# Optimization experiments

Hardware: AMD Instinct MI355X
Metric: run time of the kernel (lower is better)

## Reference

```python
import jax, jax.numpy as jnp
import numpy as np

B, S, E, L = 4, 4096, 1024, 64
SCALE = float(np.sqrt(L))


def setup_inputs() -> dict:
    key = jax.random.key(0)
    ks = jax.random.split(key, 7)
    x = jax.random.normal(ks[0], (B, S, E), dtype=jnp.float32)
    # causal mask: positions with mask==0 are disallowed (masked_fill semantics)
    mask = jnp.tril(jnp.ones((S, S), dtype=jnp.int32))
    # Linear params (torch Linear: y = x @ W.T + b); store as [E, L] for x @ W
    sd = 1.0 / np.sqrt(E)
    Wq = jax.random.uniform(ks[1], (E, L), jnp.float32, -sd, sd)
    Wk = jax.random.uniform(ks[2], (E, L), jnp.float32, -sd, sd)
    Wv = jax.random.uniform(ks[3], (E, L), jnp.float32, -sd, sd)
    bq = jax.random.uniform(ks[4], (L,), jnp.float32, -sd, sd)
    bk = jax.random.uniform(ks[5], (L,), jnp.float32, -sd, sd)
    bv = jax.random.uniform(ks[6], (L,), jnp.float32, -sd, sd)
    return {"x": x, "Wq": Wq, "Wk": Wk, "Wv": Wv,
            "bq": bq, "bk": bk, "bv": bv, "mask": mask}


def reference(x, Wq, Wk, Wv, bq, bk, bv, mask):
    # Q,K,V: [B, S, L]
    Q = x @ Wq + bq
    K = x @ Wk + bk
    V = x @ Wv + bv
    # scores: [B, S, S] -- naive full matrix, faithful to the original
    scores = jnp.einsum('bsl,btl->bst', Q, K) / SCALE
    scores = jnp.where(mask == 0, -jnp.inf, scores)
    attn = jax.nn.softmax(scores, axis=-1)
    return jnp.einsum('bst,btl->bsl', attn, V)
```

## Files before the change

### kernel.cpp

```cpp
#include <hip/hip_runtime.h>
#include <hip/hip_bf16.h>
#include <cstdint>

typedef __bf16 bf16_t;
typedef __bf16 bf16x8 __attribute__((ext_vector_type(8)));
typedef float f32x4 __attribute__((ext_vector_type(4)));

#define B_ 4
#define S_ 4096
#define E_ 1024
#define L_ 64

__device__ __forceinline__ f32x4 mfma16(bf16x8 a, bf16x8 b, f32x4 c) {
  return __builtin_amdgcn_mfma_f32_16x16x32_bf16(a, b, c, 0, 0, 0);
}

template <int CTRL>
__device__ __forceinline__ float dpp_max_step(float x) {
  int t = __builtin_amdgcn_update_dpp(0, __float_as_int(x), CTRL, 0xF, 0xF, true);
  return fmaxf(x, __int_as_float(t));
}
template <int CTRL>
__device__ __forceinline__ float dpp_add_step(float x) {
  int t = __builtin_amdgcn_update_dpp(0, __float_as_int(x), CTRL, 0xF, 0xF, true);
  return x + __int_as_float(t);
}
__device__ __forceinline__ float dpp_reduce_max16(float x) {
  x = dpp_max_step<0x121>(x);
  x = dpp_max_step<0x122>(x);
  x = dpp_max_step<0x124>(x);
  x = dpp_max_step<0x128>(x);
  return x;
}
__device__ __forceinline__ float dpp_reduce_add16(float x) {
  x = dpp_add_step<0x121>(x);
  x = dpp_add_step<0x122>(x);
  x = dpp_add_step<0x124>(x);
  x = dpp_add_step<0x128>(x);
  return x;
}


__global__ void prep_w_kernel(const float* __restrict__ Wq, const float* __restrict__ Wk,
                              const float* __restrict__ Wv, bf16_t* __restrict__ Wf) {
  int n = blockIdx.x;
  const float* W = (n < 64) ? Wq : (n < 128 ? Wk : Wv);
  int col = n & 63;
  int nt = n >> 4, lr = n & 15;
  for (int k = threadIdx.x; k < E_; k += blockDim.x) {
    int kt = k >> 5, lg = (k >> 3) & 3, e = k & 7;
    Wf[((size_t)((nt * 32 + kt) * 64 + lg * 16 + lr) << 3) + e] = (bf16_t)W[(size_t)k * L_ + col];
  }
}

__global__ __launch_bounds__(512) void qkv_proj_kernel(
    const float* __restrict__ x, const bf16_t* __restrict__ Wf,
    const float* __restrict__ bq, const float* __restrict__ bk, const float* __restrict__ bv,
    bf16_t* __restrict__ Qf, bf16_t* __restrict__ Kf, bf16_t* __restrict__ Vf) {
  __shared__ __align__(16) bf16_t xs[2][32][136];

  const int tid = threadIdx.x;
  const int w = tid >> 6, l = tid & 63;
  const int lr = l & 15, lg = l >> 4;
  const int rowgrp = w & 1, colgrp = w >> 1;
  const int m0b = blockIdx.x * 32;
  const int srow = tid >> 4, scol = (tid & 15) * 8;

  f32x4 acc[3];
#pragma unroll
  for (int t = 0; t < 3; ++t) acc[t] = f32x4{0.f, 0.f, 0.f, 0.f};

  const float* xsrc = x + (size_t)(m0b + srow) * E_ + scol;

  {
    float4 u0 = *reinterpret_cast<const float4*>(xsrc);
    float4 u1 = *reinterpret_cast<const float4*>(xsrc + 4);
    bf16x8 pk;
    pk[0] = (bf16_t)u0.x; pk[1] = (bf16_t)u0.y; pk[2] = (bf16_t)u0.z; pk[3] = (bf16_t)u0.w;
    pk[4] = (bf16_t)u1.x; pk[5] = (bf16_t)u1.y; pk[6] = (bf16_t)u1.z; pk[7] = (bf16_t)u1.w;
    *reinterpret_cast<bf16x8*>(&xs[0][srow][scol]) = pk;
  }
  float4 v0 = *reinterpret_cast<const float4*>(xsrc + 128);
  float4 v1 = *reinterpret_cast<const float4*>(xsrc + 132);
  __syncthreads();

  int buf = 0;
  for (int it = 0; it < 8; ++it) {
    if (it + 1 < 8) {
      bf16x8 pk;
      pk[0] = (bf16_t)v0.x; pk[1] = (bf16_t)v0.y; pk[2] = (bf16_t)v0.z; pk[3] = (bf16_t)v0.w;
      pk[4] = (bf16_t)v1.x; pk[5] = (bf16_t)v1.y; pk[6] = (bf16_t)v1.z; pk[7] = (bf16_t)v1.w;
      *reinterpret_cast<bf16x8*>(&xs[buf ^ 1][srow][scol]) = pk;
    }
    if (it + 2 < 8) {
      v0 = *reinterpret_cast<const float4*>(xsrc + (it + 2) * 128);
      v1 = *reinterpret_cast<const float4*>(xsrc + (it + 2) * 128 + 4);
    }
    const bf16_t* xr = &xs[buf][rowgrp * 16 + lr][0];
#pragma unroll
    for (int ks = 0; ks < 4; ++ks) {
      bf16x8 a = *reinterpret_cast<const bf16x8*>(xr + ks * 32 + lg * 8);
      const int kt = it * 4 + ks;
#pragma unroll
      for (int t = 0; t < 3; ++t) {
        const int nt = colgrp * 3 + t;
        bf16x8 b = *reinterpret_cast<const bf16x8*>(Wf + (((size_t)(nt * 32 + kt) * 64 + l) << 3));
        acc[t] = mfma16(a, b, acc[t]);
      }
    }
    __syncthreads();
    buf ^= 1;
  }

#pragma unroll
  for (int t = 0; t < 3; ++t) {
    int ng = colgrp * 48 + t * 16 + lr;
    int mat = ng >> 6;
    int ncol = ng & 63;
    const float* bias = (mat == 0) ? bq : (mat == 1 ? bk : bv);
    float bb = bias[ncol];
    const int ktq = ncol >> 5, lgw = (ncol >> 3) & 3, ew = ncol & 7;
    const int vt = ncol >> 4, lrw_v = ncol & 15;
#pragma unroll
    for (int r = 0; r < 4; ++r) {
      int mg = m0b + rowgrp * 16 + lg * 4 + r;
      float v = acc[t][r] + bb;
      if (mat < 2) {
        int rt = mg >> 4, lrw = mg & 15;
        size_t idx = (((size_t)((rt * 2 + ktq) * 64 + lgw * 16 + lrw)) << 3) + ew;
        if (mat == 0) Qf[idx] = (bf16_t)v; else Kf[idx] = (bf16_t)v;
      } else {
        int batch = mg >> 12, sl = mg & (S_ - 1);
        int st = sl >> 5, lgv = (sl >> 3) & 3, ev = sl & 7;
        Vf[((size_t)batch << 18) + (((size_t)((st * 4 + vt) * 64 + lgv * 16 + lrw_v)) << 3) + ev] = (bf16_t)v;
      }
    }
  }
}

__global__ __launch_bounds__(256) void attn_kernel(
    const bf16_t* __restrict__ Qf, const bf16_t* __restrict__ Kf,
    const bf16_t* __restrict__ Vf, float* __restrict__ Opart, float* __restrict__ mlpart) {
  __shared__ __align__(16) bf16_t p_lds[4][16 * 72];
  __shared__ bf16_t od_lds[3][16][68];
  __shared__ float ml_lds[3][16][2];

  const int c = threadIdx.x >> 6, l = threadIdx.x & 63;
  const int lr = l & 15, lg = l >> 4;
  const int u = blockIdx.x;
  const int batch = u & 3;
  const int strip = (u >> 2) & 3;
  const int h = (u >> 4) & 1;
  const int qt = 63 - (u >> 5);
  const int qsi = ((u >> 5) << 4) | (u & 15);
  const int qrow = qt * 64 + strip * 16;
  const size_t qbase = (size_t)batch * S_ + qrow;
  bf16_t* pw = p_lds[c];

  const int rtq = batch * 256 + qt * 4 + strip;
  bf16x8 qa0 = *reinterpret_cast<const bf16x8*>(Qf + (((size_t)(rtq * 2) * 64 + l) << 3));
  bf16x8 qa1 = *reinterpret_cast<const bf16x8*>(Qf + (((size_t)(rtq * 2 + 1) * 64 + l) << 3));
  const bf16_t* Vb = Vf + ((size_t)batch << 18);

  f32x4 o[4];
  float m[4], ssum[4];
#pragma unroll
  for (int rr = 0; rr < 4; ++rr) { o[rr] = f32x4{0.f, 0.f, 0.f, 0.f}; m[rr] = -1e30f; ssum[rr] = 0.f; }

  for (int kt = 2 * c + h; kt <= qt; kt += 8) {
    const int t0 = kt * 64;
    f32x4 st[4];
#pragma unroll
    for (int cf = 0; cf < 4; ++cf) st[cf] = f32x4{0.f, 0.f, 0.f, 0.f};
#pragma unroll
    for (int cf = 0; cf < 4; ++cf) {
      const int rtk = batch * 256 + kt * 4 + cf;
      bf16x8 b0 = *reinterpret_cast<const bf16x8*>(Kf + (((size_t)(rtk * 2) * 64 + l) << 3));
      bf16x8 b1 = *reinterpret_cast<const bf16x8*>(Kf + (((size_t)(rtk * 2 + 1) * 64 + l) << 3));
      st[cf] = mfma16(qa0, b0, st[cf]);
      st[cf] = mfma16(qa1, b1, st[cf]);
    }
    const bool diag = (kt == qt);
    float p[4][4];
#pragma unroll
    for (int rr = 0; rr < 4; ++rr) {
      const int qg = qrow + lg * 4 + rr;
      float rowmax = -1e30f;
#pragma unroll
      for (int cf = 0; cf < 4; ++cf) {
        float s = st[cf][rr] * 0.125f;
        if (diag && (t0 + cf * 16 + lr) > qg) s = -1e30f;
        p[cf][rr] = s;
        rowmax = fmaxf(rowmax, s);
      }
      rowmax = dpp_reduce_max16(rowmax);
      float mnew = fmaxf(m[rr], rowmax);
      float scale = __expf(m[rr] - mnew);
      float rs = 0.f;
#pragma unroll
      for (int cf = 0; cf < 4; ++cf) {
        float e = __expf(p[cf][rr] - mnew);
        p[cf][rr] = e;
        rs += e;
      }
      rs = dpp_reduce_add16(rs);
      ssum[rr] = ssum[rr] * scale + rs;
#pragma unroll
      for (int cf = 0; cf < 4; ++cf) o[cf][rr] *= scale;
      m[rr] = mnew;
    }
#pragma unroll
    for (int rr = 0; rr < 4; ++rr)
#pragma unroll
      for (int cf = 0; cf < 4; ++cf)
        pw[(lg * 4 + rr) * 72 + cf * 16 + lr] = (bf16_t)p[cf][rr];
    bf16x8 pa0 = *reinterpret_cast<const bf16x8*>(pw + lr * 72 + lg * 8);
    bf16x8 pa1 = *reinterpret_cast<const bf16x8*>(pw + lr * 72 + 32 + lg * 8);
    const int st0 = kt * 2;
#pragma unroll
    for (int cf = 0; cf < 4; ++cf) {
      bf16x8 v0 = *reinterpret_cast<const bf16x8*>(Vb + (((size_t)((st0 * 4 + cf) * 64 + l)) << 3));
      bf16x8 v1 = *reinterpret_cast<const bf16x8*>(Vb + (((size_t)(((st0 + 1) * 4 + cf) * 64 + l)) << 3));
      o[cf] = mfma16(pa0, v0, o[cf]);
      o[cf] = mfma16(pa1, v1, o[cf]);
    }
  }

  if (c > 0) {
    if (lr == 0) {
#pragma unroll
      for (int rr = 0; rr < 4; ++rr) {
        ml_lds[c - 1][lg * 4 + rr][0] = m[rr];
        ml_lds[c - 1][lg * 4 + rr][1] = ssum[rr];
      }
    }
#pragma unroll
    for (int cf = 0; cf < 4; ++cf)
#pragma unroll
      for (int rr = 0; rr < 4; ++rr)
        od_lds[c - 1][lg * 4 + rr][cf * 16 + lr] = (bf16_t)o[cf][rr];
  }
  __syncthreads();
  if (c == 0) {
    float* Op = Opart + (size_t)(h * 1024 + qsi) * 1024;
    float* mlp = mlpart + (size_t)(h * 1024 + qsi) * 32;
#pragma unroll
    for (int rr = 0; rr < 4; ++rr) {
      const int row = lg * 4 + rr;
      float M = m[rr];
      float mv[3];
#pragma unroll
      for (int cc = 0; cc < 3; ++cc) {
        mv[cc] = ml_lds[cc][row][0];
        M = fmaxf(M, mv[cc]);
      }
      float f0 = __expf(m[rr] - M);
      float Lsum = ssum[rr] * f0;
      float fc[3];
#pragma unroll
      for (int cc = 0; cc < 3; ++cc) {
        fc[cc] = __expf(mv[cc] - M);
        Lsum += ml_lds[cc][row][1] * fc[cc];
      }
      if (lr == 0) { mlp[row * 2] = M; mlp[row * 2 + 1] = Lsum; }
#pragma unroll
      for (int cf = 0; cf < 4; ++cf) {
        float val = o[cf][rr] * f0;
#pragma unroll
        for (int cc = 0; cc < 3; ++cc)
          val += (float)od_lds[cc][row][cf * 16 + lr] * fc[cc];
        Op[row * 64 + cf * 16 + lr] = val;
      }
    }
  }
}

__global__ __launch_bounds__(64) void combine_kernel(
    const float* __restrict__ Opart, const float* __restrict__ mlpart,
    float* __restrict__ out) {
  const int b = blockIdx.x;
  const int batch = b & 3, strip = (b >> 2) & 3, qt = 63 - (b >> 4);
  const int l = threadIdx.x;
  const int row = l >> 2, c0 = (l & 3) * 16;
  const float* ml0 = mlpart + ((size_t)(0 * 1024 + b) * 16 + row) * 2;
  const float* ml1 = mlpart + ((size_t)(1 * 1024 + b) * 16 + row) * 2;
  float m0 = ml0[0], l0 = ml0[1], m1 = ml1[0], l1 = ml1[1];
  float M = fmaxf(m0, m1);
  float f0 = __expf(m0 - M), f1 = __expf(m1 - M);
  float inv = 1.f / (l0 * f0 + l1 * f1);
  const float* O0 = Opart + (size_t)(0 * 1024 + b) * 1024 + row * 64 + c0;
  const float* O1 = Opart + (size_t)(1 * 1024 + b) * 1024 + row * 64 + c0;
  float* dst = out + ((size_t)batch * S_ + qt * 64 + strip * 16 + row) * L_ + c0;
#pragma unroll
  for (int j = 0; j < 4; ++j) {
    float4 a = reinterpret_cast<const float4*>(O0)[j];
    float4 bb = reinterpret_cast<const float4*>(O1)[j];
    float4 v;
    v.x = (a.x * f0 + bb.x * f1) * inv;
    v.y = (a.y * f0 + bb.y * f1) * inv;
    v.z = (a.z * f0 + bb.z * f1) * inv;
    v.w = (a.w * f0 + bb.w * f1) * inv;
    reinterpret_cast<float4*>(dst)[j] = v;
  }
}

extern "C" void kernel_launch(void* const* d_in, const int* in_sizes, int n_in,
                              void* d_out, int out_size, void* d_ws, size_t ws_size,
                              hipStream_t stream) {
  (void)in_sizes; (void)n_in; (void)out_size; (void)ws_size;
  const float* x  = (const float*)d_in[0];
  const float* Wq = (const float*)d_in[1];
  const float* Wk = (const float*)d_in[2];
  const float* Wv = (const float*)d_in[3];
  const float* bq = (const float*)d_in[4];
  const float* bk = (const float*)d_in[5];
  const float* bv = (const float*)d_in[6];
  float* out = (float*)d_out;

  char* ws = (char*)d_ws;
  bf16_t* Qf  = (bf16_t*)(ws + 0);
  bf16_t* Kf  = (bf16_t*)(ws + (size_t)2 * 1024 * 1024);
  bf16_t* Vf  = (bf16_t*)(ws + (size_t)4 * 1024 * 1024);
  bf16_t* Wf  = (bf16_t*)(ws + (size_t)6 * 1024 * 1024);
  float* Opart = (float*)(ws + (size_t)7 * 1024 * 1024);
  float* mlpart = (float*)(ws + (size_t)15 * 1024 * 1024);

  hipLaunchKernelGGL(prep_w_kernel, dim3(192), dim3(256), 0, stream, Wq, Wk, Wv, Wf);
  hipLaunchKernelGGL(qkv_proj_kernel, dim3(16384 / 32), dim3(512), 0, stream,
                     x, Wf, bq, bk, bv, Qf, Kf, Vf);
  hipLaunchKernelGGL(attn_kernel, dim3(2048), dim3(256), 0, stream,
                     Qf, Kf, Vf, Opart, mlpart);
  hipLaunchKernelGGL(combine_kernel, dim3(1024), dim3(64), 0, stream,
                     Opart, mlpart, out);
}
```

Baseline: 61.90 us.

## Stage full 64-row x tile in LDS and stage QKV output for coalesced stores

The QKV projection kernel now loads a whole 64-row by 1024 slice of x into LDS at once instead of double-buffering 32-row chunks. Each wave computes two 16-row MFMA tiles per B fragment, so every Wf load feeds two MFMAs and the grid halves. Results are staged through LDS and written as 16-byte vectors in the fragment layouts instead of scattered 2-byte stores. This gives more W reuse and coalesced writes, but uses about 132KB of LDS per block, which limits occupancy and removes the overlap between loading and compute.

```diff
diff --git a/kernel.cpp b/kernel.cpp
--- a/kernel.cpp
+++ b/kernel.cpp
@@ -57,84 +57,95 @@
     const float* __restrict__ x, const bf16_t* __restrict__ Wf,
     const float* __restrict__ bq, const float* __restrict__ bk, const float* __restrict__ bv,
     bf16_t* __restrict__ Qf, bf16_t* __restrict__ Kf, bf16_t* __restrict__ Vf) {
-  __shared__ __align__(16) bf16_t xs[2][32][136];
+  __shared__ __align__(16) char smem[64 * 1032 * 2];
+  bf16_t* xls = reinterpret_cast<bf16_t*>(smem);
+  bf16_t* stc = reinterpret_cast<bf16_t*>(smem);
 
   const int tid = threadIdx.x;
   const int w = tid >> 6, l = tid & 63;
   const int lr = l & 15, lg = l >> 4;
-  const int rowgrp = w & 1, colgrp = w >> 1;
-  const int m0b = blockIdx.x * 32;
-  const int srow = tid >> 4, scol = (tid & 15) * 8;
-
-  f32x4 acc[3];
-#pragma unroll
-  for (int t = 0; t < 3; ++t) acc[t] = f32x4{0.f, 0.f, 0.f, 0.f};
-
-  const float* xsrc = x + (size_t)(m0b + srow) * E_ + scol;
+  const int wr = w & 1, wc = w >> 1;
+  const int m0 = blockIdx.x * 64;
 
   {
-    float4 u0 = *reinterpret_cast<const float4*>(xsrc);
-    float4 u1 = *reinterpret_cast<const float4*>(xsrc + 4);
-    bf16x8 pk;
-    pk[0] = (bf16_t)u0.x; pk[1] = (bf16_t)u0.y; pk[2] = (bf16_t)u0.z; pk[3] = (bf16_t)u0.w;
-    pk[4] = (bf16_t)u1.x; pk[5] = (bf16_t)u1.y; pk[6] = (bf16_t)u1.z; pk[7] = (bf16_t)u1.w;
-    *reinterpret_cast<bf16x8*>(&xs[0][srow][scol]) = pk;
-  }
-  float4 v0 = *reinterpret_cast<const float4*>(xsrc + 128);
-  float4 v1 = *reinterpret_cast<const float4*>(xsrc + 132);
+    const int srow = tid >> 3, sc8 = tid & 7;
+    const float* src = x + (size_t)(m0 + srow) * E_;
+    bf16_t* dst = xls + srow * 1032;
+#pragma unroll
+    for (int i = 0; i < 8; ++i) {
+      const int c0 = sc8 * 16 + i * 128;
+      float4 u0 = *reinterpret_cast<const float4*>(src + c0);
+      float4 u1 = *reinterpret_cast<const float4*>(src + c0 + 4);
+      float4 u2 = *reinterpret_cast<const float4*>(src + c0 + 8);
+      float4 u3 = *reinterpret_cast<const float4*>(src + c0 + 12);
+      bf16x8 p0, p1;
+      p0[0] = (bf16_t)u0.x; p0[1] = (bf16_t)u0.y; p0[2] = (bf16_t)u0.z; p0[3] = (bf16_t)u0.w;
+      p0[4] = (bf16_t)u1.x; p0[5] = (bf16_t)u1.y; p0[6] = (bf16_t)u1.z; p0[7] = (bf16_t)u1.w;
+      p1[0] = (bf16_t)u2.x; p1[1] = (bf16_t)u2.y; p1[2] = (bf16_t)u2.z; p1[3] = (bf16_t)u2.w;
+      p1[4] = (bf16_t)u3.x; p1[5] = (bf16_t)u3.y; p1[6] = (bf16_t)u3.z; p1[7] = (bf16_t)u3.w;
+      *reinterpret_cast<bf16x8*>(dst + c0) = p0;
+      *reinterpret_cast<bf16x8*>(dst + c0 + 8) = p1;
+    }
+  }
   __syncthreads();
 
-  int buf = 0;
-  for (int it = 0; it < 8; ++it) {
-    if (it + 1 < 8) {
-      bf16x8 pk;
-      pk[0] = (bf16_t)v0.x; pk[1] = (bf16_t)v0.y; pk[2] = (bf16_t)v0.z; pk[3] = (bf16_t)v0.w;
-      pk[4] = (bf16_t)v1.x; pk[5] = (bf16_t)v1.y; pk[6] = (bf16_t)v1.z; pk[7] = (bf16_t)v1.w;
-      *reinterpret_cast<bf16x8*>(&xs[buf ^ 1][srow][scol]) = pk;
-    }
-    if (it + 2 < 8) {
-      v0 = *reinterpret_cast<const float4*>(xsrc + (it + 2) * 128);
-      v1 = *reinterpret_cast<const float4*>(xsrc + (it + 2) * 128 + 4);
-    }
-    const bf16_t* xr = &xs[buf][rowgrp * 16 + lr][0];
-#pragma unroll
-    for (int ks = 0; ks < 4; ++ks) {
-      bf16x8 a = *reinterpret_cast<const bf16x8*>(xr + ks * 32 + lg * 8);
-      const int kt = it * 4 + ks;
-#pragma unroll
-      for (int t = 0; t < 3; ++t) {
-        const int nt = colgrp * 3 + t;
-        bf16x8 b = *reinterpret_cast<const bf16x8*>(Wf + (((size_t)(nt * 32 + kt) * 64 + l) << 3));
-        acc[t] = mfma16(a, b, acc[t]);
-      }
-    }
-    __syncthreads();
-    buf ^= 1;
-  }
+  f32x4 acc[2][3];
+#pragma unroll
+  for (int at = 0; at < 2; ++at)
+#pragma unroll
+    for (int t = 0; t < 3; ++t) acc[at][t] = f32x4{0.f, 0.f, 0.f, 0.f};
+
+  const bf16_t* xa0 = xls + (size_t)(wr * 32 + lr) * 1032 + lg * 8;
+  const bf16_t* xa1 = xa0 + (size_t)16 * 1032;
+#pragma unroll 4
+  for (int kt = 0; kt < 32; ++kt) {
+    bf16x8 a0 = *reinterpret_cast<const bf16x8*>(xa0 + kt * 32);
+    bf16x8 a1 = *reinterpret_cast<const bf16x8*>(xa1 + kt * 32);
+#pragma unroll
+    for (int t = 0; t < 3; ++t) {
+      const int nt = wc * 3 + t;
+      bf16x8 b = *reinterpret_cast<const bf16x8*>(Wf + (((size_t)(nt * 32 + kt) * 64 + l) << 3));
+      acc[0][t] = mfma16(a0, b, acc[0][t]);
+      acc[1][t] = mfma16(a1, b, acc[1][t]);
+    }
+  }
+  __syncthreads();
 
 #pragma unroll
   for (int t = 0; t < 3; ++t) {
-    int ng = colgrp * 48 + t * 16 + lr;
-    int mat = ng >> 6;
-    int ncol = ng & 63;
+    const int colb = wc * 48 + t * 16;
+    const int col = colb + lr;
+    const int mat = colb >> 6;
     const float* bias = (mat == 0) ? bq : (mat == 1 ? bk : bv);
-    float bb = bias[ncol];
-    const int ktq = ncol >> 5, lgw = (ncol >> 3) & 3, ew = ncol & 7;
-    const int vt = ncol >> 4, lrw_v = ncol & 15;
-#pragma unroll
-    for (int r = 0; r < 4; ++r) {
-      int mg = m0b + rowgrp * 16 + lg * 4 + r;
-      float v = acc[t][r] + bb;
-      if (mat < 2) {
-        int rt = mg >> 4, lrw = mg & 15;
-        size_t idx = (((size_t)((rt * 2 + ktq) * 64 + lgw * 16 + lrw)) << 3) + ew;
-        if (mat == 0) Qf[idx] = (bf16_t)v; else Kf[idx] = (bf16_t)v;
-      } else {
-        int batch = mg >> 12, sl = mg & (S_ - 1);
-        int st = sl >> 5, lgv = (sl >> 3) & 3, ev = sl & 7;
-        Vf[((size_t)batch << 18) + (((size_t)((st * 4 + vt) * 64 + lgv * 16 + lrw_v)) << 3) + ev] = (bf16_t)v;
-      }
-    }
+    const float bb = bias[col & 63];
+#pragma unroll
+    for (int at = 0; at < 2; ++at)
+#pragma unroll
+      for (int r = 0; r < 4; ++r) {
+        const int row = wr * 32 + at * 16 + lg * 4 + r;
+        stc[row * 200 + col] = (bf16_t)(acc[at][t][r] + bb);
+      }
+  }
+  __syncthreads();
+
+  {
+    const int rt = tid >> 7, ktq = (tid >> 6) & 1, lane = tid & 63;
+    const int lgw = lane >> 4, lrw = lane & 15;
+    const int rtg = (m0 >> 4) + rt;
+    bf16x8 qv = *reinterpret_cast<const bf16x8*>(stc + (rt * 16 + lrw) * 200 + ktq * 32 + lgw * 8);
+    *reinterpret_cast<bf16x8*>(Qf + (((size_t)(rtg * 2 + ktq) * 64 + lane) << 3)) = qv;
+    bf16x8 kv = *reinterpret_cast<const bf16x8*>(stc + (rt * 16 + lrw) * 200 + 64 + ktq * 32 + lgw * 8);
+    *reinterpret_cast<bf16x8*>(Kf + (((size_t)(rtg * 2 + ktq) * 64 + lane) << 3)) = kv;
+    const int stl = tid >> 8, vt = (tid >> 6) & 3;
+    const int lgv = lane >> 4, lrv = lane & 15;
+    const int colv = vt * 16 + lrv;
+    bf16x8 vv;
+#pragma unroll
+    for (int e = 0; e < 8; ++e)
+      vv[e] = stc[(stl * 32 + lgv * 8 + e) * 200 + 128 + colv];
+    const int batch = m0 >> 12;
+    const int stg = ((m0 & (S_ - 1)) >> 5) + stl;
+    *reinterpret_cast<bf16x8*>(Vf + ((size_t)batch << 18) + (((size_t)(stg * 4 + vt) * 64 + lane) << 3)) = vv;
   }
 }
 
@@ -326,7 +337,7 @@
   float* mlpart = (float*)(ws + (size_t)15 * 1024 * 1024);
 
   hipLaunchKernelGGL(prep_w_kernel, dim3(192), dim3(256), 0, stream, Wq, Wk, Wv, Wf);
-  hipLaunchKernelGGL(qkv_proj_kernel, dim3(16384 / 32), dim3(512), 0, stream,
+  hipLaunchKernelGGL(qkv_proj_kernel, dim3(16384 / 64), dim3(512), 0, stream,
                      x, Wf, bq, bk, bv, Qf, Kf, Vf);
   hipLaunchKernelGGL(attn_kernel, dim3(2048), dim3(256), 0, stream,
                      Qf, Kf, Vf, Opart, mlpart);
```

After: 64.52 us. +4.2%, slower.
